# Performance work log

Measured on AMD Instinct MI355X. Metric: run time of the kernel, lower is better.

## Reference

```python
import jax, jax.numpy as jnp
import numpy as np

HIDDEN_DIM = 4096
EXPANSION = 4
SINKHORN_ITERS = 20
EPS = 1e-05
ALPHA_INIT = 0.01


def setup_inputs() -> dict:
    key = jax.random.key(0)
    k_x, k_res = jax.random.split(key)
    x = jax.random.normal(k_x, (4096, EXPANSION, HIDDEN_DIM), dtype=jnp.float32)
    rmsnorm_weight = jnp.ones((HIDDEN_DIM,), dtype=jnp.bfloat16)
    H_pre = jnp.zeros((EXPANSION,), dtype=jnp.float32)
    H_post = jnp.zeros((EXPANSION,), dtype=jnp.float32)
    H_res = ALPHA_INIT * jax.random.normal(k_res, (EXPANSION, EXPANSION), dtype=jnp.float32)
    return {"x": x, "rmsnorm_weight": rmsnorm_weight, "H_pre": H_pre,
            "H_post": H_post, "H_res": H_res}


def reference(x, rmsnorm_weight, H_pre, H_post, H_res):
    x_f32 = x.astype(jnp.float32)  # [B, n, C]
    # Pre-mix aggregation over the n expanded streams
    H_pre_act = jax.nn.sigmoid(H_pre)
    x_agg = jnp.einsum('k,bkc->bc', H_pre_act, x_f32)  # [B, C]
    # bf16 round-trip as in the original (x_agg.bfloat16().float())
    x_agg_bf = x_agg.astype(jnp.bfloat16).astype(jnp.float32)
    rms = jnp.sqrt(jnp.mean(x_agg_bf * x_agg_bf, axis=-1, keepdims=True) + EPS)
    y_norm = x_agg_bf / rms * rmsnorm_weight.astype(jnp.float32)  # [B, C]
    # Sinkhorn normalization of the tiny n x n mixing matrix
    M0 = jnp.exp(H_res.astype(jnp.float32))
    def body(M, _):
        M = M / jnp.maximum(M.sum(axis=1, keepdims=True), EPS)
        M = M / jnp.maximum(M.sum(axis=0, keepdims=True), EPS)
        return M, None
    M, _ = jax.lax.scan(body, M0, None, length=SINKHORN_ITERS)
    H_post_act = 2.0 * jax.nn.sigmoid(H_post)
    # [B, n, C]: mixed residual streams + broadcast of normalized aggregate
    out = jnp.einsum('ij,bjc->bic', M, x_f32) + H_post_act[None, :, None] * y_norm[:, None, :]
    return out
```

## Files before the change

### kernel.cpp

```cpp
#include <hip/hip_runtime.h>

constexpr int C   = 4096;
constexpr int NE  = 4;
constexpr int B   = 4096;
constexpr int THREADS = 512;
constexpr int RPB = 4;
constexpr float EPSV = 1e-5f;

__device__ inline float bf16_rne(float f) {
    unsigned int u = __float_as_uint(f);
    unsigned int r = (u + 0x7FFFu + ((u >> 16) & 1u)) & 0xFFFF0000u;
    return __uint_as_float(r);
}

__device__ __forceinline__ void ld4(const float* __restrict__ p, float (&d)[4]) {
    float4 t = *reinterpret_cast<const float4*>(p);
    d[0] = t.x; d[1] = t.y; d[2] = t.z; d[3] = t.w;
}
__device__ __forceinline__ void st4(float* __restrict__ p, const float (&d)[4]) {
    *reinterpret_cast<float4*>(p) = make_float4(d[0], d[1], d[2], d[3]);
}

__global__ __launch_bounds__(THREADS)
void mhc_pipe(const float* __restrict__ x,
              const float* __restrict__ w,
              const float* __restrict__ Hpre,
              const float* __restrict__ Hpost,
              const float* __restrict__ Hres,
              float* __restrict__ out) {
    const int tid  = threadIdx.x;
    const int lane = tid & 63;
    const int wid  = tid >> 6;
    const int cA   = wid * 256 + lane * 4;
    const int cB   = 2048 + cA;
    const size_t blockbase = (size_t)blockIdx.x * RPB * NE * C;

    __shared__ float sM[NE * NE];
    __shared__ float red[RPB][THREADS / 64];

    if (tid < 64) {
        float m = (tid < 16) ? expf(Hres[tid]) : 0.0f;
        for (int it = 0; it < 20; ++it) {
            float r = m + __shfl_xor(m, 1);
            r += __shfl_xor(r, 2);
            m /= fmaxf(r, EPSV);
            float cs = m + __shfl_xor(m, 4);
            cs += __shfl_xor(cs, 8);
            m /= fmaxf(cs, EPSV);
        }
        if (tid < 16) sM[tid] = m;
    }

    const float s0 = 1.0f / (1.0f + expf(-Hpre[0]));
    const float s1 = 1.0f / (1.0f + expf(-Hpre[1]));
    const float s2 = 1.0f / (1.0f + expf(-Hpre[2]));
    const float s3 = 1.0f / (1.0f + expf(-Hpre[3]));
    float hp[NE];
    #pragma unroll
    for (int i = 0; i < NE; ++i) hp[i] = 2.0f / (1.0f + expf(-Hpost[i]));

    float wf[2][4];
    ld4(w + cA, wf[0]);
    ld4(w + cB, wf[1]);

    float xsA[NE][2][4], xsB[NE][2][4];
    float M[NE * NE];

    auto load_row = [&](const float* __restrict__ xrow, float (&xs)[NE][2][4]) {
        #pragma unroll
        for (int k = 0; k < NE; ++k) {
            ld4(xrow + k * C + cA, xs[k][0]);
            ld4(xrow + k * C + cB, xs[k][1]);
        }
    };

    auto step = [&](int r, float (&cur)[NE][2][4], float (&nxt)[NE][2][4]) {
        float aggbf[2][4];
        float ss = 0.0f;
        #pragma unroll
        for (int h = 0; h < 2; ++h)
            #pragma unroll
            for (int e = 0; e < 4; ++e) {
                float a = s0 * cur[0][h][e] + s1 * cur[1][h][e]
                        + s2 * cur[2][h][e] + s3 * cur[3][h][e];
                float abf = bf16_rne(a);
                aggbf[h][e] = abf;
                ss += abf * abf;
            }

        #pragma unroll
        for (int off = 32; off > 0; off >>= 1) ss += __shfl_xor(ss, off);
        if (lane == 0) red[r][wid] = ss;
        __syncthreads();

        if (r == 0) {
            #pragma unroll
            for (int k = 0; k < NE * NE; ++k) M[k] = sM[k];
        }

        if (r + 1 < RPB)
            load_row(x + blockbase + (size_t)(r + 1) * NE * C, nxt);

        float tot = 0.0f;
        #pragma unroll
        for (int i = 0; i < THREADS / 64; ++i) tot += red[r][i];
        const float rinv = 1.0f / sqrtf(tot * (1.0f / (float)C) + EPSV);

        float* orow = out + blockbase + (size_t)r * NE * C;
        float y[2][4];
        #pragma unroll
        for (int h = 0; h < 2; ++h)
            #pragma unroll
            for (int e = 0; e < 4; ++e)
                y[h][e] = aggbf[h][e] * rinv * wf[h][e];

        #pragma unroll
        for (int i = 0; i < NE; ++i) {
            float o[2][4];
            #pragma unroll
            for (int h = 0; h < 2; ++h)
                #pragma unroll
                for (int e = 0; e < 4; ++e)
                    o[h][e] = M[i * NE + 0] * cur[0][h][e] + M[i * NE + 1] * cur[1][h][e]
                            + M[i * NE + 2] * cur[2][h][e] + M[i * NE + 3] * cur[3][h][e]
                            + hp[i] * y[h][e];
            st4(orow + i * C + cA, o[0]);
            st4(orow + i * C + cB, o[1]);
        }
    };

    load_row(x + blockbase, xsA);
    step(0, xsA, xsB);
    step(1, xsB, xsA);
    step(2, xsA, xsB);
    step(3, xsB, xsA);
}

extern "C" void kernel_launch(void* const* d_in, const int* in_sizes, int n_in,
                              void* d_out, int out_size, void* d_ws, size_t ws_size,
                              hipStream_t stream) {
    const float* x     = (const float*)d_in[0];
    const float* w     = (const float*)d_in[1];
    const float* Hpre  = (const float*)d_in[2];
    const float* Hpost = (const float*)d_in[3];
    const float* Hres  = (const float*)d_in[4];
    float* out         = (float*)d_out;

    mhc_pipe<<<B / RPB, THREADS, 0, stream>>>(x, w, Hpre, Hpost, Hres, out);
}
```

Measured before the change: 106.2 us.

## Process one row per 128-thread block instead of pipelined four-row blocks

Replaces the 512-thread kernel that walks four rows per block with register double-buffered prefetch by a 128-thread kernel that handles one row per block. Each thread holds eight float4 vectors per stream, reduces through two wavefronts, and recomputes the aggregate instead of keeping it in registers. The aim is more independent blocks and a shorter per-block barrier chain, relying on occupancy rather than explicit prefetch to hide memory latency. Each block still recomputes the Sinkhorn matrix, and there are now four times as many blocks, so that redundant setup work grows.

```diff
diff --git a/kernel.cpp b/kernel.cpp
--- a/kernel.cpp
+++ b/kernel.cpp
@@ -3,8 +3,8 @@
 constexpr int C   = 4096;
 constexpr int NE  = 4;
 constexpr int B   = 4096;
-constexpr int THREADS = 512;
-constexpr int RPB = 4;
+constexpr int THREADS = 128;
+constexpr int NV = C / (THREADS*4);
 constexpr float EPSV = 1e-5f;
 
 __device__ inline float bf16_rne(float f) {
@@ -17,26 +17,29 @@
     float4 t = *reinterpret_cast<const float4*>(p);
     d[0] = t.x; d[1] = t.y; d[2] = t.z; d[3] = t.w;
 }
-__device__ __forceinline__ void st4(float* __restrict__ p, const float (&d)[4]) {
-    *reinterpret_cast<float4*>(p) = make_float4(d[0], d[1], d[2], d[3]);
-}
 
 __global__ __launch_bounds__(THREADS)
-void mhc_pipe(const float* __restrict__ x,
-              const float* __restrict__ w,
-              const float* __restrict__ Hpre,
-              const float* __restrict__ Hpost,
-              const float* __restrict__ Hres,
-              float* __restrict__ out) {
+void mhc_row(const float* __restrict__ x,
+             const float* __restrict__ w,
+             const float* __restrict__ Hpre,
+             const float* __restrict__ Hpost,
+             const float* __restrict__ Hres,
+             float* __restrict__ out) {
     const int tid  = threadIdx.x;
     const int lane = tid & 63;
     const int wid  = tid >> 6;
-    const int cA   = wid * 256 + lane * 4;
-    const int cB   = 2048 + cA;
-    const size_t blockbase = (size_t)blockIdx.x * RPB * NE * C;
+    const float* xrow = x   + (size_t)blockIdx.x * NE * C;
+    float*       orow = out + (size_t)blockIdx.x * NE * C;
+
+    float xs[NE][NV][4];
+    #pragma unroll
+    for (int k = 0; k < NE; ++k)
+        #pragma unroll
+        for (int v = 0; v < NV; ++v)
+            ld4(xrow + k * C + v * (THREADS * 4) + tid * 4, xs[k][v]);
 
     __shared__ float sM[NE * NE];
-    __shared__ float red[RPB][THREADS / 64];
+    __shared__ float sred[2];
 
     if (tid < 64) {
         float m = (tid < 16) ? expf(Hres[tid]) : 0.0f;
@@ -59,81 +62,52 @@
     #pragma unroll
     for (int i = 0; i < NE; ++i) hp[i] = 2.0f / (1.0f + expf(-Hpost[i]));
 
-    float wf[2][4];
-    ld4(w + cA, wf[0]);
-    ld4(w + cB, wf[1]);
-
-    float xsA[NE][2][4], xsB[NE][2][4];
-    float M[NE * NE];
-
-    auto load_row = [&](const float* __restrict__ xrow, float (&xs)[NE][2][4]) {
+    float ss = 0.0f;
+    #pragma unroll
+    for (int v = 0; v < NV; ++v)
         #pragma unroll
-        for (int k = 0; k < NE; ++k) {
-            ld4(xrow + k * C + cA, xs[k][0]);
-            ld4(xrow + k * C + cB, xs[k][1]);
-        }
-    };
-
-    auto step = [&](int r, float (&cur)[NE][2][4], float (&nxt)[NE][2][4]) {
-        float aggbf[2][4];
-        float ss = 0.0f;
-        #pragma unroll
-        for (int h = 0; h < 2; ++h)
-            #pragma unroll
-            for (int e = 0; e < 4; ++e) {
-                float a = s0 * cur[0][h][e] + s1 * cur[1][h][e]
-                        + s2 * cur[2][h][e] + s3 * cur[3][h][e];
-                float abf = bf16_rne(a);
-                aggbf[h][e] = abf;
-                ss += abf * abf;
-            }
-
-        #pragma unroll
-        for (int off = 32; off > 0; off >>= 1) ss += __shfl_xor(ss, off);
-        if (lane == 0) red[r][wid] = ss;
-        __syncthreads();
-
-        if (r == 0) {
-            #pragma unroll
-            for (int k = 0; k < NE * NE; ++k) M[k] = sM[k];
+        for (int e = 0; e < 4; ++e) {
+            float a = s0 * xs[0][v][e] + s1 * xs[1][v][e]
+                    + s2 * xs[2][v][e] + s3 * xs[3][v][e];
+            float abf = bf16_rne(a);
+            ss += abf * abf;
         }
 
-        if (r + 1 < RPB)
-            load_row(x + blockbase + (size_t)(r + 1) * NE * C, nxt);
+    #pragma unroll
+    for (int off = 32; off > 0; off >>= 1) ss += __shfl_xor(ss, off);
+    if (lane == 0) sred[wid] = ss;
+    __syncthreads();
+    const float tot  = sred[0] + sred[1];
+    const float rinv = 1.0f / sqrtf(tot * (1.0f / (float)C) + EPSV);
 
-        float tot = 0.0f;
+    float M[NE * NE];
+    #pragma unroll
+    for (int k = 0; k < NE * NE; ++k) M[k] = sM[k];
+
+    #pragma unroll
+    for (int v = 0; v < NV; ++v) {
+        const int off = v * (THREADS * 4) + tid * 4;
+        float wf[4];
+        ld4(w + off, wf);
+        float y[4];
         #pragma unroll
-        for (int i = 0; i < THREADS / 64; ++i) tot += red[r][i];
-        const float rinv = 1.0f / sqrtf(tot * (1.0f / (float)C) + EPSV);
-
-        float* orow = out + blockbase + (size_t)r * NE * C;
-        float y[2][4];
+        for (int e = 0; e < 4; ++e) {
+            float a = s0 * xs[0][v][e] + s1 * xs[1][v][e]
+                    + s2 * xs[2][v][e] + s3 * xs[3][v][e];
+            y[e] = bf16_rne(a) * rinv * wf[e];
+        }
         #pragma unroll
-        for (int h = 0; h < 2; ++h)
+        for (int i = 0; i < NE; ++i) {
+            float o[4];
             #pragma unroll
             for (int e = 0; e < 4; ++e)
-                y[h][e] = aggbf[h][e] * rinv * wf[h][e];
-
-        #pragma unroll
-        for (int i = 0; i < NE; ++i) {
-            float o[2][4];
-            #pragma unroll
-            for (int h = 0; h < 2; ++h)
-                #pragma unroll
-                for (int e = 0; e < 4; ++e)
-                    o[h][e] = M[i * NE + 0] * cur[0][h][e] + M[i * NE + 1] * cur[1][h][e]
-                            + M[i * NE + 2] * cur[2][h][e] + M[i * NE + 3] * cur[3][h][e]
-                            + hp[i] * y[h][e];
-            st4(orow + i * C + cA, o[0]);
-            st4(orow + i * C + cB, o[1]);
+                o[e] = M[i * NE + 0] * xs[0][v][e] + M[i * NE + 1] * xs[1][v][e]
+                     + M[i * NE + 2] * xs[2][v][e] + M[i * NE + 3] * xs[3][v][e]
+                     + hp[i] * y[e];
+            *reinterpret_cast<float4*>(orow + i * C + off) =
+                make_float4(o[0], o[1], o[2], o[3]);
         }
-    };
-
-    load_row(x + blockbase, xsA);
-    step(0, xsA, xsB);
-    step(1, xsB, xsA);
-    step(2, xsA, xsB);
-    step(3, xsB, xsA);
+    }
 }
 
 extern "C" void kernel_launch(void* const* d_in, const int* in_sizes, int n_in,
@@ -146,5 +120,5 @@
     const float* Hres  = (const float*)d_in[4];
     float* out         = (float*)d_out;
 
-    mhc_pipe<<<B / RPB, THREADS, 0, stream>>>(x, w, Hpre, Hpost, Hres, out);
+    mhc_row<<<B, THREADS, 0, stream>>>(x, w, Hpre, Hpost, Hres, out);
 }
```

Result: slower. 109.9 us (+3.5%).
